# Optimization experiments

Measured on AMD Instinct MI355X. Metric: run time of the kernel, lower is better.

Reference implementation:

```python
import jax, jax.numpy as jnp
import numpy as np

DIM_HEAD = 64


def setup_inputs() -> dict:
    key = jax.random.key(0)
    ks = jax.random.split(key, 9)
    B, S, D, H, Dh = 1, 4096, 1024, 16, DIM_HEAD
    s = 0.02
    return {
        "x": jax.random.normal(ks[0], (B, S, D), jnp.float32),
        "wq": jax.random.normal(ks[1], (H, D, Dh), jnp.float32) * s,
        "bq": jax.random.normal(ks[2], (H, Dh), jnp.float32) * s,
        "wk": jax.random.normal(ks[3], (H, D, Dh), jnp.float32) * s,
        "bk": jax.random.normal(ks[4], (H, Dh), jnp.float32) * s,
        "wv": jax.random.normal(ks[5], (H, D, Dh), jnp.float32) * s,
        "bv": jax.random.normal(ks[6], (H, Dh), jnp.float32) * s,
        "wo": jax.random.normal(ks[7], (D, D), jnp.float32) * s,
        "bo": jax.random.normal(ks[8], (D,), jnp.float32) * s,
    }


def reference(x, wq, bq, wk, bk, wv, bv, wo, bo):
    # x: [B, S, D]; per-head projections batched over H (same math as
    # torch's per-head nn.Linear layers applied independently).
    B, S, D = x.shape
    H, _, Dh = wq.shape
    dot_scale = jnp.sqrt(jnp.asarray(Dh, x.dtype))
    q = jnp.einsum("bsd,hde->bhse", x, wq) + bq[None, :, None, :]  # [B,H,S,Dh]
    k = jnp.einsum("bsd,hde->bhse", x, wk) + bk[None, :, None, :]
    v = jnp.einsum("bsd,hde->bhse", x, wv) + bv[None, :, None, :]
    scores = jnp.einsum("bhse,bhte->bhst", q, k) / dot_scale        # [B,H,S,S]
    attn = jax.nn.softmax(scores, axis=-1)
    o = jnp.einsum("bhst,bhte->bhse", attn, v)                      # [B,H,S,Dh]
    # concat heads in head order -> [B, S, H*Dh]
    concat = jnp.transpose(o, (0, 2, 1, 3)).reshape(B, S, H * Dh)
    return concat @ wo + bo
```

## Files before the change

kernel.cpp:

```cpp
#include <hip/hip_runtime.h>
#include <hip/hip_bf16.h>

#define S_LEN 4096
#define DMODEL 1024
#define NHEAD 16
#define QKLD 2048

typedef __attribute__((ext_vector_type(8))) short s16x8;
typedef __attribute__((ext_vector_type(4))) float f32x4;

__device__ inline unsigned short f2bf(float f){
  unsigned u = __builtin_bit_cast(unsigned, f);
  u += 0x7FFFu + ((u >> 16) & 1u);
  return (unsigned short)(u >> 16);
}

__device__ inline float bf2f(unsigned short b){
  unsigned u = ((unsigned)b) << 16;
  return __builtin_bit_cast(float, u);
}

__device__ inline unsigned pk2bf(float a, float b){
  float2 t; t.x = a; t.y = b;
  __hip_bfloat162 h = __float22bfloat162_rn(t);
  unsigned r;
  __builtin_memcpy(&r, &h, 4);
  return r;
}

__device__ inline void gload_lds16(const void* g, void* l){
  __builtin_amdgcn_global_load_lds(
    (const __attribute__((address_space(1))) void*)g,
    (__attribute__((address_space(3))) void*)l, 16, 0, 0);
}

__global__ __launch_bounds__(256) void pack_x_kern(const float* __restrict__ x,
                                                   unsigned short* __restrict__ xb){
  int i = (blockIdx.x * 256 + threadIdx.x) * 4;
  float4 v = *(const float4*)(x + i);
  ushort4 o;
  o.x = f2bf(v.x); o.y = f2bf(v.y); o.z = f2bf(v.z); o.w = f2bf(v.w);
  *(ushort4*)(xb + i) = o;
}

__global__ __launch_bounds__(256) void pack_wqkv_kern(
    const float* __restrict__ wq, const float* __restrict__ bq,
    const float* __restrict__ wk, const float* __restrict__ bk,
    const float* __restrict__ wv, const float* __restrict__ bv,
    unsigned short* __restrict__ wt, float* __restrict__ bias){
  int idx = blockIdx.x * 256 + threadIdx.x;
  int which = idx >> 20;
  int rem = idx & 1048575;
  int e = rem & 63;
  int d = (rem >> 6) & 1023;
  int h = rem >> 16;
  const float* w = which == 0 ? wq : which == 1 ? wk : wv;
  const float* b = which == 0 ? bq : which == 1 ? bk : bv;
  float scale = which == 0 ? 0.18033688011112042f : 1.0f;
  float val = w[(h * 1024 + d) * 64 + e] * scale;
  int n = which * 1024 + h * 64 + e;
  wt[(size_t)n * 1024 + d] = f2bf(val);
  if (d == 0) bias[n] = b[h * 64 + e] * scale;
}

__global__ __launch_bounds__(256) void pack_wo_kern(const float* __restrict__ wo,
                                                    unsigned short* __restrict__ wot){
  int idx = blockIdx.x * 256 + threadIdx.x;
  int n = idx & 1023, d = idx >> 10;
  wot[(size_t)n * 1024 + d] = f2bf(wo[(size_t)d * 1024 + n]);
}

template <bool OUT_BF16, bool VFUSE>
__global__ __launch_bounds__(256) void gemm_bt(const unsigned short* __restrict__ A,
                                               const unsigned short* __restrict__ Bt,
                                               const float* __restrict__ bias,
                                               void* __restrict__ Cout,
                                               unsigned short* __restrict__ vTout,
                                               int M, int N, int K){
  __shared__ unsigned short As[128 * 64];
  __shared__ unsigned short Bs[128 * 64];
  int tid = threadIdx.x;
  int lane = tid & 63, w = tid >> 6;
  int wr = w >> 1, wc = w & 1;
  int m0 = blockIdx.y * 128, n0 = blockIdx.x * 128;
  f32x4 zero = {0.f, 0.f, 0.f, 0.f};
  f32x4 acc[4][4];
#pragma unroll
  for (int i = 0; i < 4; i++)
#pragma unroll
    for (int j = 0; j < 4; j++) acc[i][j] = zero;

  for (int ks = 0; ks < K; ks += 64){
#pragma unroll
    for (int i = 0; i < 4; i++){
      int u = i * 256 + tid;
      int row = u >> 3, c = u & 7;
      gload_lds16(A + ((size_t)(m0 + row) * K + ks + ((c ^ (row & 7)) << 3)), &As[u * 8]);
    }
#pragma unroll
    for (int i = 0; i < 4; i++){
      int u = i * 256 + tid;
      int row = u >> 3, c = u & 7;
      gload_lds16(Bt + ((size_t)(n0 + row) * K + ks + ((c ^ (row & 7)) << 3)), &Bs[u * 8]);
    }
    __syncthreads();
#pragma unroll
    for (int kk = 0; kk < 2; kk++){
      s16x8 af[4], bfr[4];
#pragma unroll
      for (int i = 0; i < 4; i++){
        int ra = wr * 64 + i * 16 + (lane & 15);
        int ca = kk * 4 + (lane >> 4);
        af[i] = *(const s16x8*)&As[ra * 64 + ((ca ^ (ra & 7)) << 3)];
        int rb = wc * 64 + i * 16 + (lane & 15);
        bfr[i] = *(const s16x8*)&Bs[rb * 64 + ((ca ^ (rb & 7)) << 3)];
      }
#pragma unroll
      for (int i = 0; i < 4; i++)
#pragma unroll
        for (int j = 0; j < 4; j++)
          acc[i][j] = __builtin_amdgcn_mfma_f32_16x16x32_bf16(af[i], bfr[j], acc[i][j], 0, 0, 0);
    }
    __syncthreads();
  }
  int g = lane >> 4;
#pragma unroll
  for (int i = 0; i < 4; i++)
#pragma unroll
    for (int j = 0; j < 4; j++){
      int col = n0 + wc * 64 + j * 16 + (lane & 15);
      float bv = bias[col];
      if (VFUSE && n0 >= 2048){
        float v0 = acc[i][j][0] + bv, v1 = acc[i][j][1] + bv;
        float v2 = acc[i][j][2] + bv, v3 = acc[i][j][3] + bv;
        uint2 pkv; pkv.x = pk2bf(v0, v1); pkv.y = pk2bf(v2, v3);
        int p0 = 32 * (i >> 1) + 8 * g + 4 * (i & 1);
        *(uint2*)&vTout[(size_t)(col - 2048) * S_LEN + m0 + wr * 64 + p0] = pkv;
      } else {
#pragma unroll
        for (int r = 0; r < 4; r++){
          int row = m0 + wr * 64 + i * 16 + 4 * g + r;
          float v = acc[i][j][r] + bv;
          if (OUT_BF16) ((unsigned short*)Cout)[(size_t)row * N + col] = f2bf(v);
          else          ((float*)Cout)[(size_t)row * N + col] = v;
        }
      }
    }
}

__global__ __launch_bounds__(256) void gemm_bt_n64(const unsigned short* __restrict__ A,
                                                   const unsigned short* __restrict__ Bt,
                                                   const float* __restrict__ bias,
                                                   float* __restrict__ Cout,
                                                   int M, int N, int K){
  __shared__ unsigned short As[128 * 64];
  __shared__ unsigned short Bs[64 * 64];
  int tid = threadIdx.x;
  int lane = tid & 63, w = tid >> 6;
  int m0 = blockIdx.y * 128, n0 = blockIdx.x * 64;
  f32x4 zero = {0.f, 0.f, 0.f, 0.f};
  f32x4 acc[2][4];
#pragma unroll
  for (int i = 0; i < 2; i++)
#pragma unroll
    for (int j = 0; j < 4; j++) acc[i][j] = zero;

  for (int ks = 0; ks < K; ks += 64){
#pragma unroll
    for (int i = 0; i < 4; i++){
      int u = i * 256 + tid;
      int row = u >> 3, c = u & 7;
      gload_lds16(A + ((size_t)(m0 + row) * K + ks + ((c ^ (row & 7)) << 3)), &As[u * 8]);
    }
#pragma unroll
    for (int i = 0; i < 2; i++){
      int u = i * 256 + tid;
      int row = u >> 3, c = u & 7;
      gload_lds16(Bt + ((size_t)(n0 + row) * K + ks + ((c ^ (row & 7)) << 3)), &Bs[u * 8]);
    }
    __syncthreads();
#pragma unroll
    for (int kk = 0; kk < 2; kk++){
      s16x8 af[2], bfr[4];
#pragma unroll
      for (int i = 0; i < 2; i++){
        int ra = w * 32 + i * 16 + (lane & 15);
        int ca = kk * 4 + (lane >> 4);
        af[i] = *(const s16x8*)&As[ra * 64 + ((ca ^ (ra & 7)) << 3)];
      }
#pragma unroll
      for (int j = 0; j < 4; j++){
        int rb = j * 16 + (lane & 15);
        int ca = kk * 4 + (lane >> 4);
        bfr[j] = *(const s16x8*)&Bs[rb * 64 + ((ca ^ (rb & 7)) << 3)];
      }
#pragma unroll
      for (int i = 0; i < 2; i++)
#pragma unroll
        for (int j = 0; j < 4; j++)
          acc[i][j] = __builtin_amdgcn_mfma_f32_16x16x32_bf16(af[i], bfr[j], acc[i][j], 0, 0, 0);
    }
    __syncthreads();
  }
  int g = lane >> 4;
#pragma unroll
  for (int i = 0; i < 2; i++)
#pragma unroll
    for (int j = 0; j < 4; j++){
      int col = n0 + j * 16 + (lane & 15);
      float bv = bias[col];
#pragma unroll
      for (int r = 0; r < 4; r++){
        int row = m0 + w * 32 + i * 16 + 4 * g + r;
        Cout[(size_t)row * N + col] = acc[i][j][r] + bv;
      }
    }
}

template <bool SPLIT>
__global__ __launch_bounds__(256) void attn_kern(const unsigned short* __restrict__ qkv,
                                                 const unsigned short* __restrict__ vT,
                                                 unsigned short* __restrict__ concat,
                                                 unsigned short* __restrict__ numpart,
                                                 float* __restrict__ lpart){
  __shared__ unsigned short lds[16384];
  int tid = threadIdx.x, lane = tid & 63, w = tid >> 6;
  int q16 = lane & 15, g = lane >> 4;
  int h = blockIdx.y;
  int z = SPLIT ? blockIdx.z : 0;
  int ntiles = SPLIT ? (S_LEN / 256) : (S_LEN / 64);
  int kt0 = z * ntiles;
  int q0 = blockIdx.x * 128 + w * 32;
  s16x8 qb[2][2];
#pragma unroll
  for (int qt = 0; qt < 2; qt++)
#pragma unroll
    for (int kk = 0; kk < 2; kk++)
      qb[qt][kk] = *(const s16x8*)&qkv[(size_t)(q0 + qt * 16 + q16) * QKLD + h * 64 + kk * 32 + g * 8];
  s16x8 ones;
#pragma unroll
  for (int j = 0; j < 8; j++) ones[j] = (short)0x3F80;
  f32x4 zero = {0.f, 0.f, 0.f, 0.f};
  f32x4 o[2][4];
  f32x4 l_acc[2];
#pragma unroll
  for (int qt = 0; qt < 2; qt++){
    l_acc[qt] = zero;
#pragma unroll
    for (int nc = 0; nc < 4; nc++) o[qt][nc] = zero;
  }
  int srow = tid >> 3, sc = tid & 7;
  int sswz = (sc ^ (srow & 7)) << 3;
  const unsigned short* kg0 = qkv + (size_t)(kt0 * 64 + srow) * QKLD + 1024 + h * 64 + sswz;
  const unsigned short* kg1 = kg0 + 32 * QKLD;
  const unsigned short* vg0 = vT + (size_t)(h * 64 + srow) * S_LEN + kt0 * 64 + sswz;
  const unsigned short* vg1 = vg0 + 32 * S_LEN;
  int d0 = tid * 8, d1 = (256 + tid) * 8;

#define STAGE(buf) do { \
    gload_lds16(kg0, &lds[(buf) * 4096 + d0]); \
    gload_lds16(vg0, &lds[8192 + (buf) * 4096 + d0]); \
    gload_lds16(kg1, &lds[(buf) * 4096 + d1]); \
    gload_lds16(vg1, &lds[8192 + (buf) * 4096 + d1]); \
    kg0 += 64 * QKLD; kg1 += 64 * QKLD; vg0 += 64; vg1 += 64; } while (0)

  STAGE(0);
  __syncthreads();
  int cur = 0;
  for (int it = 0; it < ntiles; it++){
    if (it + 1 < ntiles) STAGE(cur ^ 1);
    const unsigned short* Kc = &lds[cur * 4096];
    const unsigned short* Vc = &lds[8192 + cur * 4096];
    f32x4 s[2][4];
#pragma unroll
    for (int qt = 0; qt < 2; qt++)
#pragma unroll
      for (int ct = 0; ct < 4; ct++) s[qt][ct] = zero;
#pragma unroll
    for (int ct = 0; ct < 4; ct++)
#pragma unroll
      for (int kk = 0; kk < 2; kk++){
        int tr = ct * 16 + q16;
        int c = kk * 4 + g;
        s16x8 kf = *(const s16x8*)&Kc[tr * 64 + ((c ^ (tr & 7)) << 3)];
#pragma unroll
        for (int qt = 0; qt < 2; qt++)
          s[qt][ct] = __builtin_amdgcn_mfma_f32_16x16x32_bf16(kf, qb[qt][kk], s[qt][ct], 0, 0, 0);
      }
#pragma unroll
    for (int qt = 0; qt < 2; qt++)
#pragma unroll
      for (int ct = 0; ct < 4; ct++)
#pragma unroll
        for (int r = 0; r < 4; r++)
          s[qt][ct][r] = __builtin_amdgcn_exp2f(s[qt][ct][r]);
    s16x8 pb[2][2];
#pragma unroll
    for (int qt = 0; qt < 2; qt++)
#pragma unroll
      for (int kk = 0; kk < 2; kk++){
        union { unsigned u[4]; s16x8 v; } pk;
#pragma unroll
        for (int i = 0; i < 4; i++){
          int ct = 2 * kk + (i >> 1);
          int r = (i & 1) * 2;
          pk.u[i] = pk2bf(s[qt][ct][r], s[qt][ct][r + 1]);
        }
        pb[qt][kk] = pk.v;
      }
#pragma unroll
    for (int kk = 0; kk < 2; kk++)
#pragma unroll
      for (int qt = 0; qt < 2; qt++)
        l_acc[qt] = __builtin_amdgcn_mfma_f32_16x16x32_bf16(ones, pb[qt][kk], l_acc[qt], 0, 0, 0);
#pragma unroll
    for (int nc = 0; nc < 4; nc++)
#pragma unroll
      for (int kk = 0; kk < 2; kk++){
        int er = nc * 16 + q16;
        int c = kk * 4 + g;
        s16x8 vf = *(const s16x8*)&Vc[er * 64 + ((c ^ (er & 7)) << 3)];
#pragma unroll
        for (int qt = 0; qt < 2; qt++)
          o[qt][nc] = __builtin_amdgcn_mfma_f32_16x16x32_bf16(vf, pb[qt][kk], o[qt][nc], 0, 0, 0);
      }
    __syncthreads();
    cur ^= 1;
  }
#undef STAGE
#pragma unroll
  for (int qt = 0; qt < 2; qt++){
    size_t row = (size_t)(q0 + qt * 16 + q16);
    float l = l_acc[qt][0];
    if (SPLIT){
      if (g == 0) lpart[(size_t)z * (S_LEN * NHEAD) + row * NHEAD + h] = l;
#pragma unroll
      for (int nc = 0; nc < 4; nc++){
        uint2 pkv;
        pkv.x = pk2bf(o[qt][nc][0], o[qt][nc][1]);
        pkv.y = pk2bf(o[qt][nc][2], o[qt][nc][3]);
        *(uint2*)&numpart[(size_t)z * (S_LEN * DMODEL) + row * DMODEL + h * 64 + nc * 16 + 4 * g] = pkv;
      }
    } else {
      float inv = 1.0f / l;
#pragma unroll
      for (int nc = 0; nc < 4; nc++){
        uint2 pkv;
        pkv.x = pk2bf(o[qt][nc][0] * inv, o[qt][nc][1] * inv);
        pkv.y = pk2bf(o[qt][nc][2] * inv, o[qt][nc][3] * inv);
        *(uint2*)&concat[row * DMODEL + h * 64 + nc * 16 + 4 * g] = pkv;
      }
    }
  }
}

__global__ __launch_bounds__(256) void merge_kern(const unsigned short* __restrict__ numpart,
                                                  const float* __restrict__ lpart,
                                                  unsigned short* __restrict__ concat){
  int q = blockIdx.x, tid = threadIdx.x;
  int c = tid * 4;
  int h = c >> 6;
  float l = 0.f;
  float a0 = 0.f, a1 = 0.f, a2 = 0.f, a3 = 0.f;
#pragma unroll
  for (int z = 0; z < 4; z++){
    l += lpart[(size_t)z * (S_LEN * NHEAD) + q * NHEAD + h];
    ushort4 nv = *(const ushort4*)&numpart[(size_t)z * (S_LEN * DMODEL) + (size_t)q * DMODEL + c];
    a0 += bf2f(nv.x); a1 += bf2f(nv.y); a2 += bf2f(nv.z); a3 += bf2f(nv.w);
  }
  float inv = 1.0f / l;
  uint2 ov;
  ov.x = pk2bf(a0 * inv, a1 * inv);
  ov.y = pk2bf(a2 * inv, a3 * inv);
  *(uint2*)&concat[(size_t)q * DMODEL + c] = ov;
}

extern "C" void kernel_launch(void* const* d_in, const int* in_sizes, int n_in,
                              void* d_out, int out_size, void* d_ws, size_t ws_size,
                              hipStream_t stream){
  const float* x  = (const float*)d_in[0];
  const float* wq = (const float*)d_in[1];
  const float* bq = (const float*)d_in[2];
  const float* wk = (const float*)d_in[3];
  const float* bk = (const float*)d_in[4];
  const float* wv = (const float*)d_in[5];
  const float* bv = (const float*)d_in[6];
  const float* wo = (const float*)d_in[7];
  const float* bo = (const float*)d_in[8];
  char* ws = (char*)d_ws;
  unsigned short* xb      = (unsigned short*)(ws + 0);
  unsigned short* wqkvt   = (unsigned short*)(ws + 8388608);
  unsigned short* numpart = (unsigned short*)(ws + 0);
  unsigned short* wot     = (unsigned short*)(ws + 33554432);
  float*          biasq   = (float*)(ws + 35651584);
  unsigned short* qkv     = (unsigned short*)(ws + 35717120);
  unsigned short* vT      = (unsigned short*)(ws + 52494336);
  unsigned short* concat  = (unsigned short*)(ws + 60882944);
  float*          lpart   = (float*)(ws + 69271552);
  const size_t ws_need = 70320128;
  float* out = (float*)d_out;

  pack_x_kern<<<4096, 256, 0, stream>>>(x, xb);
  pack_wqkv_kern<<<12288, 256, 0, stream>>>(wq, bq, wk, bk, wv, bv, wqkvt, biasq);
  pack_wo_kern<<<4096, 256, 0, stream>>>(wo, wot);
  gemm_bt<true, true><<<dim3(24, 32), 256, 0, stream>>>(xb, wqkvt, biasq, qkv, vT, 4096, QKLD, 1024);
  if (ws_size >= ws_need){
    attn_kern<true><<<dim3(32, 16, 4), 256, 0, stream>>>(qkv, vT, concat, numpart, lpart);
    merge_kern<<<4096, 256, 0, stream>>>(numpart, lpart, concat);
  } else {
    attn_kern<false><<<dim3(32, 16, 1), 256, 0, stream>>>(qkv, vT, concat, numpart, lpart);
  }
  gemm_bt_n64<<<dim3(16, 32), 256, 0, stream>>>(concat, wot, bo, out, 4096, 1024, 1024);
}
```

Baseline: 182.4 us.

## Double attention block to 512 threads and remap blocks per XCD

The attention kernel now runs 8 waves per block covering 256 queries, so each staged K/V tile in shared memory is reused by twice as many query rows and each thread issues half as many staging loads. The grid is flattened to 1D, and block indices are remapped so that blocks landing on the same XCD share the same head and key split, which should improve L2 reuse of K/V. In exchange, per-block occupancy limits change and each staging wait now synchronises twice as many waves.

```diff
diff --git a/kernel.cpp b/kernel.cpp
--- a/kernel.cpp
+++ b/kernel.cpp
@@ -218,7 +218,7 @@
 }
 
 template <bool SPLIT>
-__global__ __launch_bounds__(256) void attn_kern(const unsigned short* __restrict__ qkv,
+__global__ __launch_bounds__(512) void attn_kern(const unsigned short* __restrict__ qkv,
                                                  const unsigned short* __restrict__ vT,
                                                  unsigned short* __restrict__ concat,
                                                  unsigned short* __restrict__ numpart,
@@ -226,11 +226,23 @@
   __shared__ unsigned short lds[16384];
   int tid = threadIdx.x, lane = tid & 63, w = tid >> 6;
   int q16 = lane & 15, g = lane >> 4;
-  int h = blockIdx.y;
-  int z = SPLIT ? blockIdx.z : 0;
+  int bx, h, z;
+  if (SPLIT){
+    int lin = blockIdx.x;
+    int xcd = lin & 7;
+    int m = lin >> 3;
+    int grp = xcd * 8 + (m >> 4);
+    bx = m & 15;
+    h = grp & 15;
+    z = grp >> 4;
+  } else {
+    bx = blockIdx.x & 15;
+    h = blockIdx.x >> 4;
+    z = 0;
+  }
   int ntiles = SPLIT ? (S_LEN / 256) : (S_LEN / 64);
   int kt0 = z * ntiles;
-  int q0 = blockIdx.x * 128 + w * 32;
+  int q0 = bx * 256 + w * 32;
   s16x8 qb[2][2];
 #pragma unroll
   for (int qt = 0; qt < 2; qt++)
@@ -252,17 +264,13 @@
   int srow = tid >> 3, sc = tid & 7;
   int sswz = (sc ^ (srow & 7)) << 3;
   const unsigned short* kg0 = qkv + (size_t)(kt0 * 64 + srow) * QKLD + 1024 + h * 64 + sswz;
-  const unsigned short* kg1 = kg0 + 32 * QKLD;
   const unsigned short* vg0 = vT + (size_t)(h * 64 + srow) * S_LEN + kt0 * 64 + sswz;
-  const unsigned short* vg1 = vg0 + 32 * S_LEN;
-  int d0 = tid * 8, d1 = (256 + tid) * 8;
+  int d0 = tid * 8;
 
 #define STAGE(buf) do { \
     gload_lds16(kg0, &lds[(buf) * 4096 + d0]); \
     gload_lds16(vg0, &lds[8192 + (buf) * 4096 + d0]); \
-    gload_lds16(kg1, &lds[(buf) * 4096 + d1]); \
-    gload_lds16(vg1, &lds[8192 + (buf) * 4096 + d1]); \
-    kg0 += 64 * QKLD; kg1 += 64 * QKLD; vg0 += 64; vg1 += 64; } while (0)
+    kg0 += 64 * QKLD; vg0 += 64; } while (0)
 
   STAGE(0);
   __syncthreads();
@@ -405,10 +413,10 @@
   pack_wo_kern<<<4096, 256, 0, stream>>>(wo, wot);
   gemm_bt<true, true><<<dim3(24, 32), 256, 0, stream>>>(xb, wqkvt, biasq, qkv, vT, 4096, QKLD, 1024);
   if (ws_size >= ws_need){
-    attn_kern<true><<<dim3(32, 16, 4), 256, 0, stream>>>(qkv, vT, concat, numpart, lpart);
+    attn_kern<true><<<1024, 512, 0, stream>>>(qkv, vT, concat, numpart, lpart);
     merge_kern<<<4096, 256, 0, stream>>>(numpart, lpart, concat);
   } else {
-    attn_kern<false><<<dim3(32, 16, 1), 256, 0, stream>>>(qkv, vT, concat, numpart, lpart);
+    attn_kern<false><<<256, 512, 0, stream>>>(qkv, vT, concat, numpart, lpart);
   }
   gemm_bt_n64<<<dim3(16, 32), 256, 0, stream>>>(concat, wot, bo, out, 4096, 1024, 1024);
 }
```

Measured after the change: 169.1 us. 7.3% less time.
